# Optimization experiments

Measured on AMD Instinct MI355X. Metric: run time of the kernel, lower is better.

Reference implementation:

```python
import jax, jax.numpy as jnp
import numpy as np

HIDDEN = 1024
HEADS = 16
D_K = HIDDEN // HEADS
B, S = 2, 2048


def setup_inputs() -> dict:
    key = jax.random.key(0)
    ks = jax.random.split(key, 11)
    sc = 1.0 / np.sqrt(HIDDEN)
    return {
        "query": jax.random.normal(ks[0], (B, S, HIDDEN), jnp.float32),
        "key": jax.random.normal(ks[1], (B, S, HIDDEN), jnp.float32),
        "value": jax.random.normal(ks[2], (B, S, HIDDEN), jnp.float32),
        "w_q": jax.random.normal(ks[3], (HIDDEN, HIDDEN), jnp.float32) * sc,
        "b_q": jax.random.normal(ks[4], (HIDDEN,), jnp.float32) * 0.02,
        "w_k": jax.random.normal(ks[5], (HIDDEN, HIDDEN), jnp.float32) * sc,
        "b_k": jax.random.normal(ks[6], (HIDDEN,), jnp.float32) * 0.02,
        "w_v": jax.random.normal(ks[7], (HIDDEN, HIDDEN), jnp.float32) * sc,
        "b_v": jax.random.normal(ks[8], (HIDDEN,), jnp.float32) * 0.02,
        "w_o": jax.random.normal(ks[9], (HIDDEN, HIDDEN), jnp.float32) * sc,
        "b_o": jax.random.normal(ks[10], (HIDDEN,), jnp.float32) * 0.02,
    }


def reference(query, key, value, w_q, b_q, w_k, b_k, w_v, b_v, w_o, b_o):
    b, s, _ = query.shape
    # linear projections (torch Linear: x @ W^T + b)
    q = query @ w_q.T + b_q
    k = key @ w_k.T + b_k
    v = value @ w_v.T + b_v
    # [B, H, S, D]
    q = q.reshape(b, s, HEADS, D_K).transpose(0, 2, 1, 3)
    k = k.reshape(b, s, HEADS, D_K).transpose(0, 2, 1, 3)
    v = v.reshape(b, s, HEADS, D_K).transpose(0, 2, 1, 3)
    scale = jnp.float32(1.0 / np.sqrt(D_K))
    scores = jnp.einsum('bhqd,bhkd->bhqk', q, k) * scale  # [B,H,S,S]
    probs = jax.nn.softmax(scores, axis=-1)
    y = jnp.einsum('bhqk,bhkd->bhqd', probs, v)
    y = y.transpose(0, 2, 1, 3).reshape(b, s, HIDDEN)
    return y @ w_o.T + b_o
```

## Files before the change

kernel.cpp:

```cpp
#include <hip/hip_runtime.h>
#include <hip/hip_bf16.h>
#include <math.h>

#define HIDDEN 1024
#define HEADS 16
#define DK 64
#define BB 2
#define SS 2048
#define MROWS (BB*SS)

typedef __attribute__((ext_vector_type(8))) short short8;
typedef __attribute__((ext_vector_type(4))) float f32x4;
typedef __attribute__((ext_vector_type(4))) unsigned short ushort4_t;

static __device__ __forceinline__ unsigned short f2bf(float f) {
    unsigned int u = __float_as_uint(f);
    u += 0x7fffu + ((u >> 16) & 1u);
    return (unsigned short)(u >> 16);
}

__global__ __launch_bounds__(256) void cast_all(
    const float* __restrict__ q, const float* __restrict__ k, const float* __restrict__ v,
    const float* __restrict__ wq, const float* __restrict__ wk,
    const float* __restrict__ wv, const float* __restrict__ wo,
    unsigned short* __restrict__ Xq, unsigned short* __restrict__ Xk, unsigned short* __restrict__ Xv,
    unsigned short* __restrict__ Wq, unsigned short* __restrict__ Wk,
    unsigned short* __restrict__ Wv, unsigned short* __restrict__ Wo) {
    int i = blockIdx.x * 256 + threadIdx.x;
    const float* src; unsigned short* dst; int off;
    if (i < (3 << 20)) {
        int w = i >> 20; off = i & ((1 << 20) - 1);
        src = (w == 0) ? q : (w == 1) ? k : v;
        dst = (w == 0) ? Xq : (w == 1) ? Xk : Xv;
    } else {
        int j = i - (3 << 20);
        int w = j >> 18; off = j & ((1 << 18) - 1);
        src = (w == 0) ? wq : (w == 1) ? wk : (w == 2) ? wv : wo;
        dst = (w == 0) ? Wq : (w == 1) ? Wk : (w == 2) ? Wv : Wo;
    }
    float4 f = reinterpret_cast<const float4*>(src)[off];
    ushort4_t o;
    o.x = f2bf(f.x); o.y = f2bf(f.y); o.z = f2bf(f.z); o.w = f2bf(f.w);
    reinterpret_cast<ushort4_t*>(dst)[off] = o;
}

__global__ __launch_bounds__(256, 3) void gemm_qkv(
    const unsigned short* __restrict__ Xq, const unsigned short* __restrict__ Xk, const unsigned short* __restrict__ Xv,
    const unsigned short* __restrict__ Wq, const unsigned short* __restrict__ Wk, const unsigned short* __restrict__ Wv,
    const float* __restrict__ bq, const float* __restrict__ bk, const float* __restrict__ bv,
    unsigned short* __restrict__ Qb, unsigned short* __restrict__ Kb, unsigned short* __restrict__ Vt,
    float scale_q) {
    __shared__ unsigned short As[128][40];
    __shared__ unsigned short Bs[128][40];
    const int z = blockIdx.z;
    const unsigned short* A  = (z == 0) ? Xq : (z == 1) ? Xk : Xv;
    const unsigned short* Wt = (z == 0) ? Wq : (z == 1) ? Wk : Wv;
    const float* bias        = (z == 0) ? bq : (z == 1) ? bk : bv;
    unsigned short* O        = (z == 0) ? Qb : (z == 1) ? Kb : Vt;
    const float oscale       = (z == 0) ? scale_q : 1.0f;

    const int t    = threadIdx.x;
    const int lane = t & 63;
    const int wave = t >> 6;
    const int m0 = blockIdx.y * 128;
    const int n0 = blockIdx.x * 128;
    const int row  = t >> 2;
    const int col8 = (t & 3) * 8;

    const int wm = (wave >> 1) * 64;
    const int wn = (wave & 1) * 64;
    const int lr = lane & 15;
    const int lk = (lane >> 4) * 8;

    f32x4 acc[4][4];
#pragma unroll
    for (int i = 0; i < 4; i++)
#pragma unroll
        for (int j = 0; j < 4; j++) acc[i][j] = f32x4{0.f, 0.f, 0.f, 0.f};

    for (int k0 = 0; k0 < HIDDEN; k0 += 32) {
        short8 av0 = *reinterpret_cast<const short8*>(A  + (size_t)(m0 + row)      * HIDDEN + k0 + col8);
        short8 av1 = *reinterpret_cast<const short8*>(A  + (size_t)(m0 + row + 64) * HIDDEN + k0 + col8);
        short8 bv0 = *reinterpret_cast<const short8*>(Wt + (size_t)(n0 + row)      * HIDDEN + k0 + col8);
        short8 bv1 = *reinterpret_cast<const short8*>(Wt + (size_t)(n0 + row + 64) * HIDDEN + k0 + col8);
        __syncthreads();
        *reinterpret_cast<short8*>(&As[row][col8])      = av0;
        *reinterpret_cast<short8*>(&As[row + 64][col8]) = av1;
        *reinterpret_cast<short8*>(&Bs[row][col8])      = bv0;
        *reinterpret_cast<short8*>(&Bs[row + 64][col8]) = bv1;
        __syncthreads();
        short8 af[4], bfr[4];
#pragma unroll
        for (int i = 0; i < 4; i++) af[i]  = *reinterpret_cast<const short8*>(&As[wm + i * 16 + lr][lk]);
#pragma unroll
        for (int j = 0; j < 4; j++) bfr[j] = *reinterpret_cast<const short8*>(&Bs[wn + j * 16 + lr][lk]);
#pragma unroll
        for (int i = 0; i < 4; i++)
#pragma unroll
            for (int j = 0; j < 4; j++)
                acc[i][j] = __builtin_amdgcn_mfma_f32_16x16x32_bf16(af[i], bfr[j], acc[i][j], 0, 0, 0);
    }

#pragma unroll
    for (int i = 0; i < 4; i++) {
        int mrow = m0 + wm + i * 16 + (lane >> 4) * 4;
#pragma unroll
        for (int j = 0; j < 4; j++) {
            int ncol = n0 + wn + j * 16 + lr;
            float bv = bias[ncol];
            int b_ = mrow >> 11;
            int h_ = ncol >> 6;
            int d_ = ncol & 63;
            if (z != 2) {
#pragma unroll
                for (int r = 0; r < 4; r++) {
                    int s_ = (mrow + r) & 2047;
                    O[(((size_t)(b_ * HEADS + h_)) * SS + s_) * DK + d_] = f2bf((acc[i][j][r] + bv) * oscale);
                }
            } else {
                int s0 = mrow & 2047;
                ushort4_t pk;
                pk.x = f2bf(acc[i][j][0] + bv);
                pk.y = f2bf(acc[i][j][1] + bv);
                pk.z = f2bf(acc[i][j][2] + bv);
                pk.w = f2bf(acc[i][j][3] + bv);
                *reinterpret_cast<ushort4_t*>(O + (((size_t)(b_ * HEADS + h_) * DK + d_) * SS + s0)) = pk;
            }
        }
    }
}

__global__ __launch_bounds__(256) void gemm_o(const unsigned short* __restrict__ A,
                                              const unsigned short* __restrict__ Wt,
                                              const float* __restrict__ bias,
                                              float* __restrict__ O) {
    __shared__ unsigned short As[128][40];
    __shared__ unsigned short Bs[64][40];
    const int t    = threadIdx.x;
    const int lane = t & 63;
    const int wave = t >> 6;
    const int m0 = blockIdx.y * 128;
    const int n0 = blockIdx.x * 64;
    const int row  = t >> 2;
    const int col8 = (t & 3) * 8;

    const int wm = wave * 32;
    const int lr = lane & 15;
    const int lk = (lane >> 4) * 8;

    f32x4 acc[2][4];
#pragma unroll
    for (int i = 0; i < 2; i++)
#pragma unroll
        for (int j = 0; j < 4; j++) acc[i][j] = f32x4{0.f, 0.f, 0.f, 0.f};

    for (int k0 = 0; k0 < HIDDEN; k0 += 32) {
        short8 av0 = *reinterpret_cast<const short8*>(A  + (size_t)(m0 + row)      * HIDDEN + k0 + col8);
        short8 av1 = *reinterpret_cast<const short8*>(A  + (size_t)(m0 + row + 64) * HIDDEN + k0 + col8);
        short8 bv0 = *reinterpret_cast<const short8*>(Wt + (size_t)(n0 + row)      * HIDDEN + k0 + col8);
        __syncthreads();
        *reinterpret_cast<short8*>(&As[row][col8])      = av0;
        *reinterpret_cast<short8*>(&As[row + 64][col8]) = av1;
        *reinterpret_cast<short8*>(&Bs[row][col8])      = bv0;
        __syncthreads();
        short8 af[2], bfr[4];
#pragma unroll
        for (int i = 0; i < 2; i++) af[i]  = *reinterpret_cast<const short8*>(&As[wm + i * 16 + lr][lk]);
#pragma unroll
        for (int j = 0; j < 4; j++) bfr[j] = *reinterpret_cast<const short8*>(&Bs[j * 16 + lr][lk]);
#pragma unroll
        for (int i = 0; i < 2; i++)
#pragma unroll
            for (int j = 0; j < 4; j++)
                acc[i][j] = __builtin_amdgcn_mfma_f32_16x16x32_bf16(af[i], bfr[j], acc[i][j], 0, 0, 0);
    }

#pragma unroll
    for (int i = 0; i < 2; i++) {
        int mrow = m0 + wm + i * 16 + (lane >> 4) * 4;
#pragma unroll
        for (int j = 0; j < 4; j++) {
            int ncol = n0 + j * 16 + lr;
            float bv = bias[ncol];
#pragma unroll
            for (int r = 0; r < 4; r++)
                O[(size_t)(mrow + r) * HIDDEN + ncol] = acc[i][j][r] + bv;
        }
    }
}

__global__ __launch_bounds__(256, 3) void attn_kernel(const unsigned short* __restrict__ Qb,
                                                      const unsigned short* __restrict__ Kb,
                                                      const unsigned short* __restrict__ Vt,
                                                      unsigned short* __restrict__ Yb) {
    __shared__ __attribute__((aligned(16))) unsigned short Ksh[2][64 * 64];
    __shared__ __attribute__((aligned(16))) unsigned short Vsh[2][64 * 64];
    __shared__ __attribute__((aligned(16))) unsigned short Psh[4][32][64];

    const int t    = threadIdx.x;
    const int lane = t & 63;
    const int wave = t >> 6;
    const int bh = blockIdx.y;
    const int b_ = bh >> 4, h_ = bh & 15;
    const int qbase = blockIdx.x * 128 + wave * 32;
    const unsigned short* Qp = Qb + (size_t)bh * SS * DK;
    const unsigned short* Kp = Kb + (size_t)bh * SS * DK;
    const unsigned short* Vp = Vt + (size_t)bh * DK * SS;
    const int lr = lane & 15;
    const int g  = lane >> 4;

    const int sr = lane >> 3;
    const int cs = (lane & 7) ^ sr;

    short8 bq[2][2];
#pragma unroll
    for (int qh = 0; qh < 2; qh++)
#pragma unroll
        for (int dh = 0; dh < 2; dh++)
            bq[qh][dh] = *reinterpret_cast<const short8*>(
                Qp + (size_t)(qbase + qh * 16 + lr) * DK + dh * 32 + g * 8);

    f32x4 accd[4][2];
#pragma unroll
    for (int dt = 0; dt < 4; dt++)
#pragma unroll
        for (int qh = 0; qh < 2; qh++) accd[dt][qh] = f32x4{0.f, 0.f, 0.f, 0.f};
    float mi[2] = {-INFINITY, -INFINITY};
    float li[2] = {0.f, 0.f};

#define STAGE(BUF, KV0) do {                                                                 \
    __builtin_amdgcn_global_load_lds(                                                        \
        (const __attribute__((address_space(1))) unsigned int*)(Kp + (size_t)((KV0) + wave * 16 + sr) * DK + cs * 8), \
        (__attribute__((address_space(3))) unsigned int*)&Ksh[BUF][(wave * 16) * 64], 16, 0, 0); \
    __builtin_amdgcn_global_load_lds(                                                        \
        (const __attribute__((address_space(1))) unsigned int*)(Kp + (size_t)((KV0) + wave * 16 + 8 + sr) * DK + cs * 8), \
        (__attribute__((address_space(3))) unsigned int*)&Ksh[BUF][(wave * 16 + 8) * 64], 16, 0, 0); \
    __builtin_amdgcn_global_load_lds(                                                        \
        (const __attribute__((address_space(1))) unsigned int*)(Vp + (size_t)(wave * 16 + sr) * SS + (KV0) + cs * 8), \
        (__attribute__((address_space(3))) unsigned int*)&Vsh[BUF][(wave * 16) * 64], 16, 0, 0); \
    __builtin_amdgcn_global_load_lds(                                                        \
        (const __attribute__((address_space(1))) unsigned int*)(Vp + (size_t)(wave * 16 + 8 + sr) * SS + (KV0) + cs * 8), \
        (__attribute__((address_space(3))) unsigned int*)&Vsh[BUF][(wave * 16 + 8) * 64], 16, 0, 0); \
} while (0)

    STAGE(0, 0);
    __syncthreads();

    for (int kv0 = 0; kv0 < SS; kv0 += 64) {
        const int cur = (kv0 >> 6) & 1;
        if (kv0 + 64 < SS) STAGE(cur ^ 1, kv0 + 64);

        short8 kf[4][2];
#pragma unroll
        for (int tt = 0; tt < 4; tt++)
#pragma unroll
            for (int h = 0; h < 2; h++)
                kf[tt][h] = *reinterpret_cast<const short8*>(
                    &Ksh[cur][(tt * 16 + lr) * 64 + (((h * 4 + g) ^ (lr & 7)) << 3)]);

        f32x4 sv[2][4];
#pragma unroll
        for (int qh = 0; qh < 2; qh++)
#pragma unroll
            for (int tt = 0; tt < 4; tt++) {
                f32x4 z = f32x4{0.f, 0.f, 0.f, 0.f};
                z = __builtin_amdgcn_mfma_f32_16x16x32_bf16(kf[tt][0], bq[qh][0], z, 0, 0, 0);
                z = __builtin_amdgcn_mfma_f32_16x16x32_bf16(kf[tt][1], bq[qh][1], z, 0, 0, 0);
                sv[qh][tt] = z;
            }

#pragma unroll
        for (int qh = 0; qh < 2; qh++) {
            float vmax = sv[qh][0][0];
#pragma unroll
            for (int tt = 0; tt < 4; tt++)
#pragma unroll
                for (int r = 0; r < 4; r++) vmax = fmaxf(vmax, sv[qh][tt][r]);
            vmax = fmaxf(vmax, __shfl_xor(vmax, 16));
            vmax = fmaxf(vmax, __shfl_xor(vmax, 32));
            if (!__all(vmax <= mi[qh] + 8.0f)) {
                float mnew = fmaxf(mi[qh], vmax);
                float sc = __builtin_amdgcn_exp2f(mi[qh] - mnew);
                li[qh] *= sc;
#pragma unroll
                for (int dt = 0; dt < 4; dt++)
#pragma unroll
                    for (int r = 0; r < 4; r++) accd[dt][qh][r] *= sc;
                mi[qh] = mnew;
            }
            float p[16];
            float rs = 0.f;
#pragma unroll
            for (int tt = 0; tt < 4; tt++)
#pragma unroll
                for (int r = 0; r < 4; r++) {
                    p[tt * 4 + r] = __builtin_amdgcn_exp2f(sv[qh][tt][r] - mi[qh]);
                    rs += p[tt * 4 + r];
                }
            rs += __shfl_xor(rs, 16);
            rs += __shfl_xor(rs, 32);
            li[qh] += rs;
#pragma unroll
            for (int tt = 0; tt < 4; tt++) {
                ushort4_t pk;
                pk.x = f2bf(p[tt * 4 + 0]);
                pk.y = f2bf(p[tt * 4 + 1]);
                pk.z = f2bf(p[tt * 4 + 2]);
                pk.w = f2bf(p[tt * 4 + 3]);
                int cw = (2 * tt + (g >> 1)) ^ (lr & 7);
                *reinterpret_cast<ushort4_t*>(&Psh[wave][qh * 16 + lr][cw * 8 + (g & 1) * 4]) = pk;
            }
        }

        __builtin_amdgcn_sched_barrier(0);

        short8 pf[2][2];
#pragma unroll
        for (int qh = 0; qh < 2; qh++)
#pragma unroll
            for (int h = 0; h < 2; h++)
                pf[qh][h] = *reinterpret_cast<const short8*>(
                    &Psh[wave][qh * 16 + lr][((h * 4 + g) ^ (lr & 7)) * 8]);

#pragma unroll
        for (int dt = 0; dt < 4; dt++) {
            short8 vf0 = *reinterpret_cast<const short8*>(
                &Vsh[cur][(dt * 16 + lr) * 64 + ((g ^ (lr & 7)) << 3)]);
            short8 vf1 = *reinterpret_cast<const short8*>(
                &Vsh[cur][(dt * 16 + lr) * 64 + (((4 + g) ^ (lr & 7)) << 3)]);
#pragma unroll
            for (int qh = 0; qh < 2; qh++) {
                accd[dt][qh] = __builtin_amdgcn_mfma_f32_16x16x32_bf16(vf0, pf[qh][0], accd[dt][qh], 0, 0, 0);
                accd[dt][qh] = __builtin_amdgcn_mfma_f32_16x16x32_bf16(vf1, pf[qh][1], accd[dt][qh], 0, 0, 0);
            }
        }
        __syncthreads();
    }
#undef STAGE

    float inv[2] = {1.0f / li[0], 1.0f / li[1]};
#pragma unroll
    for (int qh = 0; qh < 2; qh++) {
        size_t ob = ((size_t)b_ * SS + qbase + qh * 16 + lr) * HIDDEN + h_ * 64 + g * 4;
#pragma unroll
        for (int dt = 0; dt < 4; dt++) {
            ushort4_t o;
            o.x = f2bf(accd[dt][qh][0] * inv[qh]);
            o.y = f2bf(accd[dt][qh][1] * inv[qh]);
            o.z = f2bf(accd[dt][qh][2] * inv[qh]);
            o.w = f2bf(accd[dt][qh][3] * inv[qh]);
            *reinterpret_cast<ushort4_t*>(Yb + ob + dt * 16) = o;
        }
    }
}

extern "C" void kernel_launch(void* const* d_in, const int* in_sizes, int n_in,
                              void* d_out, int out_size, void* d_ws, size_t ws_size,
                              hipStream_t stream) {
    const float* query = (const float*)d_in[0];
    const float* key_  = (const float*)d_in[1];
    const float* value = (const float*)d_in[2];
    const float* w_q = (const float*)d_in[3];
    const float* b_q = (const float*)d_in[4];
    const float* w_k = (const float*)d_in[5];
    const float* b_k = (const float*)d_in[6];
    const float* w_v = (const float*)d_in[7];
    const float* b_v = (const float*)d_in[8];
    const float* w_o = (const float*)d_in[9];
    const float* b_o = (const float*)d_in[10];

    const size_t SZ_X = (size_t)MROWS * HIDDEN * 2;
    const size_t SZ_W = (size_t)HIDDEN * HIDDEN * 2;
    char* ws = (char*)d_ws;
    unsigned short* Xq = (unsigned short*)(ws);
    unsigned short* Xk = (unsigned short*)(ws + SZ_X);
    unsigned short* Xv = (unsigned short*)(ws + 2 * SZ_X);
    unsigned short* Wq = (unsigned short*)(ws + 3 * SZ_X);
    unsigned short* Wk = (unsigned short*)(ws + 3 * SZ_X + SZ_W);
    unsigned short* Wv = (unsigned short*)(ws + 3 * SZ_X + 2 * SZ_W);
    unsigned short* Wo = (unsigned short*)(ws + 3 * SZ_X + 3 * SZ_W);
    unsigned short* Qb = (unsigned short*)(ws + 3 * SZ_X + 4 * SZ_W);
    unsigned short* Kbf = (unsigned short*)(ws + 4 * SZ_X + 4 * SZ_W);
    unsigned short* Vt  = (unsigned short*)(ws + 5 * SZ_X + 4 * SZ_W);
    unsigned short* Yb  = (unsigned short*)(ws + 6 * SZ_X + 4 * SZ_W);

    cast_all<<<16384, 256, 0, stream>>>(query, key_, value, w_q, w_k, w_v, w_o,
                                        Xq, Xk, Xv, Wq, Wk, Wv, Wo);

    const float SCALE_Q = 0.125f * 1.4426950408889634f;
    gemm_qkv<<<dim3(HIDDEN / 128, MROWS / 128, 3), 256, 0, stream>>>(
        Xq, Xk, Xv, Wq, Wk, Wv, b_q, b_k, b_v, Qb, Kbf, Vt, SCALE_Q);

    attn_kernel<<<dim3(SS / 128, BB * HEADS), 256, 0, stream>>>(Qb, Kbf, Vt, Yb);

    gemm_o<<<dim3(HIDDEN / 64, MROWS / 128), 256, 0, stream>>>(Yb, Wo, b_o, (float*)d_out);
}
```

Baseline: 148.0 us.

## Remap block orders for XCD locality, shrink attention blocks, fuse Wo cast

Several changes land together. The QKV and output GEMMs get a swizzled block-id mapping so neighbouring blocks on the same XCD share A bands. The attention kernel drops to 128 threads with 64 queries per block and a head-interleaved grid mapping. It also stops staging V in LDS and loads V fragments straight from global memory into registers. The W_o bf16 conversion moves out of the cast kernel into gemm_o, and packed v_cvt_pk_bf16_f32 conversions are added. The risks are global-load latency on V inside the inner loop and redundant conversion of W_o across row blocks.

```diff
diff --git a/kernel.cpp b/kernel.cpp
--- a/kernel.cpp
+++ b/kernel.cpp
@@ -19,13 +19,17 @@
     return (unsigned short)(u >> 16);
 }
 
+static __device__ __forceinline__ unsigned int cvtpk(float lo, float hi) {
+    unsigned int r;
+    asm volatile("v_cvt_pk_bf16_f32 %0, %1, %2" : "=v"(r) : "v"(lo), "v"(hi));
+    return r;
+}
+
 __global__ __launch_bounds__(256) void cast_all(
     const float* __restrict__ q, const float* __restrict__ k, const float* __restrict__ v,
-    const float* __restrict__ wq, const float* __restrict__ wk,
-    const float* __restrict__ wv, const float* __restrict__ wo,
+    const float* __restrict__ wq, const float* __restrict__ wk, const float* __restrict__ wv,
     unsigned short* __restrict__ Xq, unsigned short* __restrict__ Xk, unsigned short* __restrict__ Xv,
-    unsigned short* __restrict__ Wq, unsigned short* __restrict__ Wk,
-    unsigned short* __restrict__ Wv, unsigned short* __restrict__ Wo) {
+    unsigned short* __restrict__ Wq, unsigned short* __restrict__ Wk, unsigned short* __restrict__ Wv) {
     int i = blockIdx.x * 256 + threadIdx.x;
     const float* src; unsigned short* dst; int off;
     if (i < (3 << 20)) {
@@ -35,8 +39,8 @@
     } else {
         int j = i - (3 << 20);
         int w = j >> 18; off = j & ((1 << 18) - 1);
-        src = (w == 0) ? wq : (w == 1) ? wk : (w == 2) ? wv : wo;
-        dst = (w == 0) ? Wq : (w == 1) ? Wk : (w == 2) ? Wv : Wo;
+        src = (w == 0) ? wq : (w == 1) ? wk : wv;
+        dst = (w == 0) ? Wq : (w == 1) ? Wk : Wv;
     }
     float4 f = reinterpret_cast<const float4*>(src)[off];
     ushort4_t o;
@@ -52,18 +56,23 @@
     float scale_q) {
     __shared__ unsigned short As[128][40];
     __shared__ unsigned short Bs[128][40];
-    const int z = blockIdx.z;
+    const int lid = blockIdx.x + 8 * (blockIdx.y + 32 * blockIdx.z);
+    const int c = lid & 7, i2 = lid >> 3;
+    const int nb = i2 & 7;
+    const int band = c * 12 + (i2 >> 3);
+    const int yb = band & 31;
+    const int z  = band >> 5;
     const unsigned short* A  = (z == 0) ? Xq : (z == 1) ? Xk : Xv;
     const unsigned short* Wt = (z == 0) ? Wq : (z == 1) ? Wk : Wv;
-    const float* bias        = (z == 0) ? bq : (z == 1) ? bk : bv;
-    unsigned short* O        = (z == 0) ? Qb : (z == 1) ? Kb : Vt;
-    const float oscale       = (z == 0) ? scale_q : 1.0f;
+    const float* bias = (z == 0) ? bq : (z == 1) ? bk : bv;
+    unsigned short* O = (z == 0) ? Qb : (z == 1) ? Kb : Vt;
+    const float oscale = (z == 0) ? scale_q : 1.0f;
 
     const int t    = threadIdx.x;
     const int lane = t & 63;
     const int wave = t >> 6;
-    const int m0 = blockIdx.y * 128;
-    const int n0 = blockIdx.x * 128;
+    const int m0 = yb * 128;
+    const int n0 = nb * 128;
     const int row  = t >> 2;
     const int col8 = (t & 3) * 8;
 
@@ -107,7 +116,7 @@
 #pragma unroll
         for (int j = 0; j < 4; j++) {
             int ncol = n0 + wn + j * 16 + lr;
-            float bv = bias[ncol];
+            float bvv = bias[ncol];
             int b_ = mrow >> 11;
             int h_ = ncol >> 6;
             int d_ = ncol & 63;
@@ -115,15 +124,15 @@
 #pragma unroll
                 for (int r = 0; r < 4; r++) {
                     int s_ = (mrow + r) & 2047;
-                    O[(((size_t)(b_ * HEADS + h_)) * SS + s_) * DK + d_] = f2bf((acc[i][j][r] + bv) * oscale);
+                    O[(((size_t)(b_ * HEADS + h_)) * SS + s_) * DK + d_] = f2bf((acc[i][j][r] + bvv) * oscale);
                 }
             } else {
                 int s0 = mrow & 2047;
                 ushort4_t pk;
-                pk.x = f2bf(acc[i][j][0] + bv);
-                pk.y = f2bf(acc[i][j][1] + bv);
-                pk.z = f2bf(acc[i][j][2] + bv);
-                pk.w = f2bf(acc[i][j][3] + bv);
+                pk.x = f2bf(acc[i][j][0] + bvv);
+                pk.y = f2bf(acc[i][j][1] + bvv);
+                pk.z = f2bf(acc[i][j][2] + bvv);
+                pk.w = f2bf(acc[i][j][3] + bvv);
                 *reinterpret_cast<ushort4_t*>(O + (((size_t)(b_ * HEADS + h_) * DK + d_) * SS + s0)) = pk;
             }
         }
@@ -131,16 +140,20 @@
 }
 
 __global__ __launch_bounds__(256) void gemm_o(const unsigned short* __restrict__ A,
-                                              const unsigned short* __restrict__ Wt,
+                                              const float* __restrict__ Wt,
                                               const float* __restrict__ bias,
                                               float* __restrict__ O) {
     __shared__ unsigned short As[128][40];
     __shared__ unsigned short Bs[64][40];
+    const int lid = blockIdx.x + 16 * blockIdx.y;
+    const int c = lid & 7, i2 = lid >> 3;
+    const int nb = i2 & 15;
+    const int band = c * 4 + (i2 >> 4);
     const int t    = threadIdx.x;
     const int lane = t & 63;
     const int wave = t >> 6;
-    const int m0 = blockIdx.y * 128;
-    const int n0 = blockIdx.x * 64;
+    const int m0 = band * 128;
+    const int n0 = nb * 64;
     const int row  = t >> 2;
     const int col8 = (t & 3) * 8;
 
@@ -155,13 +168,22 @@
         for (int j = 0; j < 4; j++) acc[i][j] = f32x4{0.f, 0.f, 0.f, 0.f};
 
     for (int k0 = 0; k0 < HIDDEN; k0 += 32) {
-        short8 av0 = *reinterpret_cast<const short8*>(A  + (size_t)(m0 + row)      * HIDDEN + k0 + col8);
-        short8 av1 = *reinterpret_cast<const short8*>(A  + (size_t)(m0 + row + 64) * HIDDEN + k0 + col8);
-        short8 bv0 = *reinterpret_cast<const short8*>(Wt + (size_t)(n0 + row)      * HIDDEN + k0 + col8);
+        short8 av0 = *reinterpret_cast<const short8*>(A + (size_t)(m0 + row)      * HIDDEN + k0 + col8);
+        short8 av1 = *reinterpret_cast<const short8*>(A + (size_t)(m0 + row + 64) * HIDDEN + k0 + col8);
+        const float* w0 = Wt + (size_t)(n0 + row) * HIDDEN + k0 + col8;
+        float4 w00 = reinterpret_cast<const float4*>(w0)[0];
+        float4 w01 = reinterpret_cast<const float4*>(w0)[1];
         __syncthreads();
         *reinterpret_cast<short8*>(&As[row][col8])      = av0;
         *reinterpret_cast<short8*>(&As[row + 64][col8]) = av1;
-        *reinterpret_cast<short8*>(&Bs[row][col8])      = bv0;
+        {
+            union { unsigned int u[4]; short8 s; } pk;
+            pk.u[0] = cvtpk(w00.x, w00.y);
+            pk.u[1] = cvtpk(w00.z, w00.w);
+            pk.u[2] = cvtpk(w01.x, w01.y);
+            pk.u[3] = cvtpk(w01.z, w01.w);
+            *reinterpret_cast<short8*>(&Bs[row][col8]) = pk.s;
+        }
         __syncthreads();
         short8 af[2], bfr[4];
 #pragma unroll
@@ -181,34 +203,34 @@
 #pragma unroll
         for (int j = 0; j < 4; j++) {
             int ncol = n0 + j * 16 + lr;
-            float bv = bias[ncol];
+            float bvv = bias[ncol];
 #pragma unroll
             for (int r = 0; r < 4; r++)
-                O[(size_t)(mrow + r) * HIDDEN + ncol] = acc[i][j][r] + bv;
+                O[(size_t)(mrow + r) * HIDDEN + ncol] = acc[i][j][r] + bvv;
         }
     }
 }
 
-__global__ __launch_bounds__(256, 3) void attn_kernel(const unsigned short* __restrict__ Qb,
+__global__ __launch_bounds__(128, 2) void attn_kernel(const unsigned short* __restrict__ Qb,
                                                       const unsigned short* __restrict__ Kb,
                                                       const unsigned short* __restrict__ Vt,
                                                       unsigned short* __restrict__ Yb) {
     __shared__ __attribute__((aligned(16))) unsigned short Ksh[2][64 * 64];
-    __shared__ __attribute__((aligned(16))) unsigned short Vsh[2][64 * 64];
-    __shared__ __attribute__((aligned(16))) unsigned short Psh[4][32][64];
+    __shared__ __attribute__((aligned(16))) unsigned short Psh[2][32][64];
 
     const int t    = threadIdx.x;
     const int lane = t & 63;
     const int wave = t >> 6;
-    const int bh = blockIdx.y;
+    const int fid  = blockIdx.y * gridDim.x + blockIdx.x;
+    const int qblk = (fid >> 3) & 31;
+    const int bh   = (fid & 7) * 4 + (fid >> 8);
     const int b_ = bh >> 4, h_ = bh & 15;
-    const int qbase = blockIdx.x * 128 + wave * 32;
+    const int qbase = qblk * 64 + wave * 32;
     const unsigned short* Qp = Qb + (size_t)bh * SS * DK;
     const unsigned short* Kp = Kb + (size_t)bh * SS * DK;
     const unsigned short* Vp = Vt + (size_t)bh * DK * SS;
     const int lr = lane & 15;
     const int g  = lane >> 4;
-
     const int sr = lane >> 3;
     const int cs = (lane & 7) ^ sr;
 
@@ -228,27 +250,20 @@
     float mi[2] = {-INFINITY, -INFINITY};
     float li[2] = {0.f, 0.f};
 
-#define STAGE(BUF, KV0) do {                                                                 \
-    __builtin_amdgcn_global_load_lds(                                                        \
-        (const __attribute__((address_space(1))) unsigned int*)(Kp + (size_t)((KV0) + wave * 16 + sr) * DK + cs * 8), \
-        (__attribute__((address_space(3))) unsigned int*)&Ksh[BUF][(wave * 16) * 64], 16, 0, 0); \
-    __builtin_amdgcn_global_load_lds(                                                        \
-        (const __attribute__((address_space(1))) unsigned int*)(Kp + (size_t)((KV0) + wave * 16 + 8 + sr) * DK + cs * 8), \
-        (__attribute__((address_space(3))) unsigned int*)&Ksh[BUF][(wave * 16 + 8) * 64], 16, 0, 0); \
-    __builtin_amdgcn_global_load_lds(                                                        \
-        (const __attribute__((address_space(1))) unsigned int*)(Vp + (size_t)(wave * 16 + sr) * SS + (KV0) + cs * 8), \
-        (__attribute__((address_space(3))) unsigned int*)&Vsh[BUF][(wave * 16) * 64], 16, 0, 0); \
-    __builtin_amdgcn_global_load_lds(                                                        \
-        (const __attribute__((address_space(1))) unsigned int*)(Vp + (size_t)(wave * 16 + 8 + sr) * SS + (KV0) + cs * 8), \
-        (__attribute__((address_space(3))) unsigned int*)&Vsh[BUF][(wave * 16 + 8) * 64], 16, 0, 0); \
+#define STAGEK(BUF, KV0) do {                                                                \
+    _Pragma("unroll")                                                                        \
+    for (int j = 0; j < 4; j++)                                                              \
+        __builtin_amdgcn_global_load_lds(                                                    \
+            (const __attribute__((address_space(1))) unsigned int*)(Kp + (size_t)((KV0) + wave * 32 + j * 8 + sr) * DK + cs * 8), \
+            (__attribute__((address_space(3))) unsigned int*)&Ksh[BUF][(wave * 32 + j * 8) * 64], 16, 0, 0); \
 } while (0)
 
-    STAGE(0, 0);
+    STAGEK(0, 0);
     __syncthreads();
 
     for (int kv0 = 0; kv0 < SS; kv0 += 64) {
         const int cur = (kv0 >> 6) & 1;
-        if (kv0 + 64 < SS) STAGE(cur ^ 1, kv0 + 64);
+        if (kv0 + 64 < SS) STAGEK(cur ^ 1, kv0 + 64);
 
         short8 kf[4][2];
 #pragma unroll
@@ -257,6 +272,14 @@
             for (int h = 0; h < 2; h++)
                 kf[tt][h] = *reinterpret_cast<const short8*>(
                     &Ksh[cur][(tt * 16 + lr) * 64 + (((h * 4 + g) ^ (lr & 7)) << 3)]);
+
+        short8 vv[4][2];
+#pragma unroll
+        for (int dt = 0; dt < 4; dt++)
+#pragma unroll
+            for (int h2 = 0; h2 < 2; h2++)
+                vv[dt][h2] = *reinterpret_cast<const short8*>(
+                    Vp + (size_t)(dt * 16 + lr) * SS + kv0 + h2 * 32 + g * 8);
 
         f32x4 sv[2][4];
 #pragma unroll
@@ -302,13 +325,11 @@
             li[qh] += rs;
 #pragma unroll
             for (int tt = 0; tt < 4; tt++) {
-                ushort4_t pk;
-                pk.x = f2bf(p[tt * 4 + 0]);
-                pk.y = f2bf(p[tt * 4 + 1]);
-                pk.z = f2bf(p[tt * 4 + 2]);
-                pk.w = f2bf(p[tt * 4 + 3]);
+                union { unsigned int u[2]; ushort4_t s; } pk;
+                pk.u[0] = cvtpk(p[tt * 4 + 0], p[tt * 4 + 1]);
+                pk.u[1] = cvtpk(p[tt * 4 + 2], p[tt * 4 + 3]);
                 int cw = (2 * tt + (g >> 1)) ^ (lr & 7);
-                *reinterpret_cast<ushort4_t*>(&Psh[wave][qh * 16 + lr][cw * 8 + (g & 1) * 4]) = pk;
+                *reinterpret_cast<ushort4_t*>(&Psh[wave][qh * 16 + lr][cw * 8 + (g & 1) * 4]) = pk.s;
             }
         }
 
@@ -323,20 +344,15 @@
                     &Psh[wave][qh * 16 + lr][((h * 4 + g) ^ (lr & 7)) * 8]);
 
 #pragma unroll
-        for (int dt = 0; dt < 4; dt++) {
-            short8 vf0 = *reinterpret_cast<const short8*>(
-                &Vsh[cur][(dt * 16 + lr) * 64 + ((g ^ (lr & 7)) << 3)]);
-            short8 vf1 = *reinterpret_cast<const short8*>(
-                &Vsh[cur][(dt * 16 + lr) * 64 + (((4 + g) ^ (lr & 7)) << 3)]);
+        for (int dt = 0; dt < 4; dt++)
 #pragma unroll
             for (int qh = 0; qh < 2; qh++) {
-                accd[dt][qh] = __builtin_amdgcn_mfma_f32_16x16x32_bf16(vf0, pf[qh][0], accd[dt][qh], 0, 0, 0);
-                accd[dt][qh] = __builtin_amdgcn_mfma_f32_16x16x32_bf16(vf1, pf[qh][1], accd[dt][qh], 0, 0, 0);
+                accd[dt][qh] = __builtin_amdgcn_mfma_f32_16x16x32_bf16(vv[dt][0], pf[qh][0], accd[dt][qh], 0, 0, 0);
+                accd[dt][qh] = __builtin_amdgcn_mfma_f32_16x16x32_bf16(vv[dt][1], pf[qh][1], accd[dt][qh], 0, 0, 0);
             }
-        }
         __syncthreads();
     }
-#undef STAGE
+#undef STAGEK
 
     float inv[2] = {1.0f / li[0], 1.0f / li[1]};
 #pragma unroll
@@ -378,20 +394,19 @@
     unsigned short* Wq = (unsigned short*)(ws + 3 * SZ_X);
     unsigned short* Wk = (unsigned short*)(ws + 3 * SZ_X + SZ_W);
     unsigned short* Wv = (unsigned short*)(ws + 3 * SZ_X + 2 * SZ_W);
-    unsigned short* Wo = (unsigned short*)(ws + 3 * SZ_X + 3 * SZ_W);
-    unsigned short* Qb = (unsigned short*)(ws + 3 * SZ_X + 4 * SZ_W);
-    unsigned short* Kbf = (unsigned short*)(ws + 4 * SZ_X + 4 * SZ_W);
-    unsigned short* Vt  = (unsigned short*)(ws + 5 * SZ_X + 4 * SZ_W);
-    unsigned short* Yb  = (unsigned short*)(ws + 6 * SZ_X + 4 * SZ_W);
-
-    cast_all<<<16384, 256, 0, stream>>>(query, key_, value, w_q, w_k, w_v, w_o,
-                                        Xq, Xk, Xv, Wq, Wk, Wv, Wo);
+    unsigned short* Qb  = (unsigned short*)(ws + 3 * SZ_X + 3 * SZ_W);
+    unsigned short* Kbf = (unsigned short*)(ws + 4 * SZ_X + 3 * SZ_W);
+    unsigned short* Vt  = (unsigned short*)(ws + 5 * SZ_X + 3 * SZ_W);
+    unsigned short* Yb  = (unsigned short*)(ws + 6 * SZ_X + 3 * SZ_W);
+
+    cast_all<<<15360, 256, 0, stream>>>(query, key_, value, w_q, w_k, w_v,
+                                        Xq, Xk, Xv, Wq, Wk, Wv);
 
     const float SCALE_Q = 0.125f * 1.4426950408889634f;
-    gemm_qkv<<<dim3(HIDDEN / 128, MROWS / 128, 3), 256, 0, stream>>>(
+    gemm_qkv<<<dim3(8, 32, 3), 256, 0, stream>>>(
         Xq, Xk, Xv, Wq, Wk, Wv, b_q, b_k, b_v, Qb, Kbf, Vt, SCALE_Q);
 
-    attn_kernel<<<dim3(SS / 128, BB * HEADS), 256, 0, stream>>>(Qb, Kbf, Vt, Yb);
-
-    gemm_o<<<dim3(HIDDEN / 64, MROWS / 128), 256, 0, stream>>>(Yb, Wo, b_o, (float*)d_out);
-}
+    attn_kernel<<<dim3(32, 32), 128, 0, stream>>>(Qb, Kbf, Vt, Yb);
+
+    gemm_o<<<dim3(16, 32), 256, 0, stream>>>(Yb, w_o, b_o, (float*)d_out);
+}
```

Result: slower. 156.5 us (+5.8%).
